# Kernel tuning notes

Hardware: AMD Instinct MI355X
Metric: run time of the kernel (lower is better)

## Reference

```python
import jax, jax.numpy as jnp
import numpy as np

H, C = 8, 32          # heads, per-head channels
N, E = 100000, 1600000
NEG_SLOPE = 0.2
LN_EPS = 1e-5


def layer_norm(x, g, b):
    mu = jnp.mean(x, axis=-1, keepdims=True)
    var = jnp.mean((x - mu) ** 2, axis=-1, keepdims=True)
    return (x - mu) * jax.lax.rsqrt(var + LN_EPS) * g + b


def setup_inputs() -> dict:
    key = jax.random.key(0)
    ks = jax.random.split(key, 8)
    x = jax.random.normal(ks[0], (N, C), dtype=jnp.float32)
    edge_index = jax.random.randint(ks[1], (2, E), 0, N, dtype=jnp.int64)
    s = 1.0 / np.sqrt(C)
    W_gat = jax.random.normal(ks[2], (C, H * C), dtype=jnp.float32) * s
    att_src = jax.random.normal(ks[3], (H, C), dtype=jnp.float32) * s
    att_dst = jax.random.normal(ks[4], (H, C), dtype=jnp.float32) * s
    bias_gat = jnp.zeros((C,), jnp.float32)
    w1 = jax.random.normal(ks[5], (C, 128), dtype=jnp.float32) * s
    b1 = jnp.zeros((128,), jnp.float32)
    w2 = jax.random.normal(ks[6], (128, C), dtype=jnp.float32) / np.sqrt(128)
    b2 = jnp.zeros((C,), jnp.float32)
    g1 = jnp.ones((C,), jnp.float32); be1 = jnp.zeros((C,), jnp.float32)
    g2 = jnp.ones((C,), jnp.float32); be2 = jnp.zeros((C,), jnp.float32)
    return dict(x=x, edge_index=edge_index, W_gat=W_gat, att_src=att_src,
                att_dst=att_dst, bias_gat=bias_gat, w1=w1, b1=b1, w2=w2,
                b2=b2, g1=g1, be1=be1, g2=g2, be2=be2)


def gat_conv(x, edge_index, W_gat, att_src, att_dst, bias_gat):
    n = x.shape[0]
    # add self loops (PyG default)
    loops = jnp.arange(n, dtype=edge_index.dtype)
    ei = jnp.concatenate([edge_index, jnp.stack([loops, loops])], axis=1)
    src, dst = ei[0], ei[1]
    xp = (x @ W_gat).reshape(n, H, C)                      # [N,H,C]
    a_src = jnp.einsum('nhc,hc->nh', xp, att_src)          # [N,H]
    a_dst = jnp.einsum('nhc,hc->nh', xp, att_dst)
    alpha = jax.nn.leaky_relu(a_src[src] + a_dst[dst], NEG_SLOPE)  # [E',H]
    # segment softmax over incoming edges of each dst node
    m = jax.ops.segment_max(alpha, dst, num_segments=n)
    ea = jnp.exp(alpha - m[dst])
    denom = jax.ops.segment_sum(ea, dst, num_segments=n)
    attn = ea / (denom[dst] + 1e-16)                       # [E',H]
    msg = xp[src] * attn[..., None]                        # [E',H,C]
    out = jax.ops.segment_sum(msg, dst, num_segments=n)    # [N,H,C]
    return out.mean(axis=1) + bias_gat                     # concat=False -> head mean


def reference(x, edge_index, W_gat, att_src, att_dst, bias_gat,
              w1, b1, w2, b2, g1, be1, g2, be2):
    h = gat_conv(x, edge_index, W_gat, att_src, att_dst, bias_gat)
    h = layer_norm(h + x, g1, be1)
    ff = jax.nn.relu(h @ w1 + b1) @ w2 + b2
    return layer_norm(ff + h, g2, be2)
```

## Files before the change

### kernel.cpp

```cpp
#include <hip/hip_runtime.h>
#include <hip/hip_fp16.h>
#include <stdint.h>

#define HH 8
#define CC 32
#define HC 256
#define FF 128
#define NEG 0.2f
#define LNEPS 1e-5f

typedef __attribute__((ext_vector_type(8))) short bf16x8;
typedef __attribute__((ext_vector_type(4))) float f32x4;
typedef unsigned short u16;

__device__ inline unsigned bf16r(float f) {
  unsigned u = __float_as_uint(f);
  return (u + 0x7fffu + ((u >> 16) & 1u)) >> 16;
}
__device__ inline float bflo(unsigned w) { return __uint_as_float(w << 16); }
__device__ inline float bfhi(unsigned w) { return __uint_as_float(w & 0xffff0000u); }
__device__ inline float leaky(float v) { return v >= 0.f ? v : NEG * v; }
__device__ inline float h2f(unsigned hbits) {
  return __half2float(__ushort_as_half((unsigned short)hbits));
}
__device__ inline u16 f2h(float f) {
  return __half_as_ushort(__float2half(f));
}
__device__ inline float ub0(unsigned w) { return (float)(w & 0xffu); }
__device__ inline float ub1(unsigned w) { return (float)((w >> 8) & 0xffu); }
__device__ inline float ub2(unsigned w) { return (float)((w >> 16) & 0xffu); }
__device__ inline float ub3(unsigned w) { return (float)(w >> 24); }

__global__ __launch_bounds__(256) void klayout(
    const float* __restrict__ W, const float* __restrict__ atts,
    const float* __restrict__ attd, const float* __restrict__ w1,
    const float* __restrict__ w2,
    u16* __restrict__ Wb, u16* __restrict__ Zb,
    u16* __restrict__ V1b, u16* __restrict__ V2b)
{
  int t = threadIdx.x;
  for (int i = t; i < 16 * 512; i += 256) {
    int j = i & 7, l = (i >> 3) & 63, nb = i >> 9;
    int k = 8 * (l >> 4) + j, c = 16 * nb + (l & 15);
    Wb[i] = (u16)bf16r(W[k * HC + c]);
  }
  for (int i = t; i < 8 * 512; i += 256) {
    int j = i & 7, l = (i >> 3) & 63, kb = i >> 9;
    int k = 32 * kb + 8 * (l >> 4) + j;
    int tc = l & 15;
    float v = 0.f;
    if (tc < 8)  { if ((k >> 5) == tc)     v = atts[tc * 32 + (k & 31)]; }
    else         { if ((k >> 5) == tc - 8) v = attd[(tc - 8) * 32 + (k & 31)]; }
    Zb[i] = (u16)bf16r(v);
  }
  for (int i = t; i < 8 * 512; i += 256) {
    int j = i & 7, l = (i >> 3) & 63, nb = i >> 9;
    int k = 8 * (l >> 4) + j, c = 16 * nb + (l & 15);
    V1b[i] = (u16)bf16r(w1[k * FF + c]);
  }
  for (int i = t; i < 8 * 512; i += 256) {
    int j = i & 7, l = (i >> 3) & 63, kn = i >> 9;
    int kb = kn >> 1, nb2 = kn & 1;
    int k = 32 * kb + 8 * (l >> 4) + j, c = 16 * nb2 + (l & 15);
    V2b[i] = (u16)bf16r(w2[k * CC + c]);
  }
}

__global__ __launch_bounds__(256) void k1m(
    const float* __restrict__ x, const u16* __restrict__ Wb,
    const u16* __restrict__ Zb, const int* __restrict__ ei,
    unsigned* __restrict__ xq8, unsigned* __restrict__ ascp,
    float* __restrict__ a_d, int* __restrict__ deg,
    unsigned* __restrict__ dstr, int n, int e, int nbc)
{
  if ((int)blockIdx.x >= nbc) {
    int i = ((int)blockIdx.x - nbc) * 1024 + (int)threadIdx.x * 4;
    if (i >= e) return;
    const int* dst = ei + e;
    if (i + 3 < e) {
      int4 d4 = *(const int4*)(dst + i);
      unsigned r0 = (unsigned)atomicAdd(&deg[d4.x], 1);
      unsigned r1 = (unsigned)atomicAdd(&deg[d4.y], 1);
      unsigned r2 = (unsigned)atomicAdd(&deg[d4.z], 1);
      unsigned r3 = (unsigned)atomicAdd(&deg[d4.w], 1);
      uint4 o;
      o.x = (unsigned)d4.x | (r0 << 17);
      o.y = (unsigned)d4.y | (r1 << 17);
      o.z = (unsigned)d4.z | (r2 << 17);
      o.w = (unsigned)d4.w | (r3 << 17);
      *(uint4*)(dstr + i) = o;
    } else {
      for (int k = 0; k < 4 && i + k < e; ++k) {
        int d = dst[i + k];
        unsigned r = (unsigned)atomicAdd(&deg[d], 1);
        dstr[i + k] = (unsigned)d | (r << 17);
      }
    }
    return;
  }
  __shared__ u16 lt[4][16 * 264];
  __shared__ float lsc[4][16][8];
  int wid = threadIdx.x >> 6, lane = threadIdx.x & 63;
  int q = lane & 15, g = lane >> 4;
  long node0 = (long)((int)blockIdx.x * 4 + wid) * 16;
  if (node0 + 16 > n) node0 = n - 16;
  u16* L = lt[wid];

  const float* xr = x + (node0 + q) * CC + 8 * g;
  float4 xa = *(const float4*)xr, xb = *(const float4*)(xr + 4);
  bf16x8 af;
  af[0] = (short)bf16r(xa.x); af[1] = (short)bf16r(xa.y);
  af[2] = (short)bf16r(xa.z); af[3] = (short)bf16r(xa.w);
  af[4] = (short)bf16r(xb.x); af[5] = (short)bf16r(xb.y);
  af[6] = (short)bf16r(xb.z); af[7] = (short)bf16r(xb.w);

#pragma unroll
  for (int nb = 0; nb < 16; ++nb) {
    bf16x8 bf = *(const bf16x8*)(Wb + nb * 512 + lane * 8);
    f32x4 acc = {0.f, 0.f, 0.f, 0.f};
    acc = __builtin_amdgcn_mfma_f32_16x16x32_bf16(af, bf, acc, 0, 0, 0);
    int col = 16 * nb + q;
#pragma unroll
    for (int r = 0; r < 4; ++r)
      L[(4 * g + r) * 264 + col] = (u16)bf16r(acc[r]);
  }
  __syncthreads();

  f32x4 az = {0.f, 0.f, 0.f, 0.f};
#pragma unroll
  for (int kb = 0; kb < 8; ++kb) {
    bf16x8 a2 = *(const bf16x8*)(L + q * 264 + kb * 32 + g * 8);
    bf16x8 zb = *(const bf16x8*)(Zb + kb * 512 + lane * 8);
    az = __builtin_amdgcn_mfma_f32_16x16x32_bf16(a2, zb, az, 0, 0, 0);
  }
  int hq = q & 7;
  u16* ascp16 = (u16*)ascp;
  if (q < 8) {
#pragma unroll
    for (int r = 0; r < 4; ++r)
      ascp16[((node0 + 4 * g + r) * HH + hq) * 2] = (u16)bf16r(az[r]);
  } else {
#pragma unroll
    for (int r = 0; r < 4; ++r)
      a_d[(node0 + 4 * g + r) * HH + hq] = az[r];
  }

#pragma unroll
  for (int t2 = 0; t2 < 2; ++t2) {
    int task = t2 * 64 + lane;
    int r = task >> 3, h = task & 7;
    const unsigned* p = (const unsigned*)(L + r * 264 + h * 32);
    float mx = 0.f;
#pragma unroll
    for (int i = 0; i < 16; ++i) {
      unsigned w = p[i];
      mx = fmaxf(mx, fmaxf(fabsf(bflo(w)), fabsf(bfhi(w))));
    }
    float rinv = (mx > 0.f) ? 127.f / mx : 0.f;
    ascp16[((node0 + r) * HH + h) * 2 + 1] = f2h(mx * (1.f / 127.f));
    lsc[wid][r][h] = rinv;
  }
  __syncthreads();

#pragma unroll
  for (int i = 0; i < 16; ++i) {
    int d = i * 64 + lane;
    int r = d >> 6, c = d & 63;
    int h = c >> 3;
    float rv = lsc[wid][r][h];
    const unsigned* p = (const unsigned*)(L + r * 264) + (c << 1);
    unsigned w0 = p[0], w1 = p[1];
    int q0 = __float2int_rn(bflo(w0) * rv);
    int q1 = __float2int_rn(bfhi(w0) * rv);
    int q2 = __float2int_rn(bflo(w1) * rv);
    int q3 = __float2int_rn(bfhi(w1) * rv);
    q0 = min(max(q0, -127), 127) + 128;
    q1 = min(max(q1, -127), 127) + 128;
    q2 = min(max(q2, -127), 127) + 128;
    q3 = min(max(q3, -127), 127) + 128;
    unsigned pk = (unsigned)q0 | ((unsigned)q1 << 8) |
                  ((unsigned)q2 << 16) | ((unsigned)q3 << 24);
    xq8[(node0 + r) * 64 + c] = pk;
  }
}

__global__ __launch_bounds__(256) void kscanA(const int* __restrict__ deg,
                                              int* __restrict__ bsum, int n)
{
  __shared__ int ws[4];
  int t = threadIdx.x;
  int i = (int)blockIdx.x * 1024 + t * 4;
  int4 v = make_int4(0, 0, 0, 0);
  if (i + 3 < n) v = *(const int4*)(deg + i);
  else {
    if (i     < n) v.x = deg[i];
    if (i + 1 < n) v.y = deg[i + 1];
    if (i + 2 < n) v.z = deg[i + 2];
    if (i + 3 < n) v.w = deg[i + 3];
  }
  int s = v.x + v.y + v.z + v.w;
#pragma unroll
  for (int mask = 1; mask < 64; mask <<= 1) s += __shfl_xor(s, mask);
  if ((t & 63) == 0) ws[t >> 6] = s;
  __syncthreads();
  if (t == 0) bsum[blockIdx.x] = ws[0] + ws[1] + ws[2] + ws[3];
}

__global__ __launch_bounds__(1024) void kscanB(int* __restrict__ bsum, int nb)
{
  __shared__ int wsum[16];
  int t = threadIdx.x, lane = t & 63, wid = t >> 6;
  int v = (t < nb) ? bsum[t] : 0;
  int s = v;
#pragma unroll
  for (int d = 1; d < 64; d <<= 1) { int tt = __shfl_up(s, d); if (lane >= d) s += tt; }
  if (lane == 63) wsum[wid] = s;
  __syncthreads();
  if (wid == 0) {
    int w = (lane < 16) ? wsum[lane] : 0;
#pragma unroll
    for (int d = 1; d < 16; d <<= 1) { int tt = __shfl_up(w, d); if (lane >= d) w += tt; }
    if (lane < 16) wsum[lane] = w;
  }
  __syncthreads();
  int excl = s - v + ((wid > 0) ? wsum[wid - 1] : 0);
  if (t < nb) bsum[t] = excl;
}

__global__ __launch_bounds__(256) void kscanC(const int* __restrict__ deg,
                                              const int* __restrict__ bsum,
                                              int* __restrict__ offs, int n)
{
  __shared__ int ws[4];
  int t = threadIdx.x, lane = t & 63, wid = t >> 6;
  int i = (int)blockIdx.x * 1024 + t * 4;
  int4 v = make_int4(0, 0, 0, 0);
  if (i + 3 < n) v = *(const int4*)(deg + i);
  else {
    if (i     < n) v.x = deg[i];
    if (i + 1 < n) v.y = deg[i + 1];
    if (i + 2 < n) v.z = deg[i + 2];
    if (i + 3 < n) v.w = deg[i + 3];
  }
  int tsum = v.x + v.y + v.z + v.w;
  int s = tsum;
#pragma unroll
  for (int d = 1; d < 64; d <<= 1) { int tt = __shfl_up(s, d); if (lane >= d) s += tt; }
  if (lane == 63) ws[wid] = s;
  __syncthreads();
  if (t == 0) {
    int a = ws[0]; ws[0] = 0;
    int b = ws[1]; ws[1] = a; a += b;
    int c = ws[2]; ws[2] = a; a += c;
    ws[3] = a;
  }
  __syncthreads();
  int base = bsum[blockIdx.x] + ws[wid] + (s - tsum);
  if (i     < n) offs[i]     = base; base += v.x;
  if (i + 1 < n) offs[i + 1] = base; base += v.y;
  if (i + 2 < n) offs[i + 2] = base; base += v.z;
  if (i + 3 < n) offs[i + 3] = base;
}

__global__ __launch_bounds__(256) void kscatter(
    const int* __restrict__ ei, const unsigned* __restrict__ dstr, int e,
    const int* __restrict__ offs, int* __restrict__ csr, int n)
{
  int oct = (int)blockIdx.x & 3;
  int nsub = (int)gridDim.x >> 2;
  int sub = (int)blockIdx.x >> 2;
  int nper = (n + 3) >> 2;
  int lo = oct * nper, hi = lo + nper;
  int stride = nsub << 10;
  for (int i = (sub * 256 + (int)threadIdx.x) * 4; i < e; i += stride) {
    if (i + 3 < e) {
      uint4 d4 = *(const uint4*)(dstr + i);
      int4 s4 = *(const int4*)(ei + i);
      int dx = d4.x & 0x1ffff, dy = d4.y & 0x1ffff,
          dz = d4.z & 0x1ffff, dw = d4.w & 0x1ffff;
      if (dx >= lo && dx < hi) csr[offs[dx] + (d4.x >> 17)] = s4.x;
      if (dy >= lo && dy < hi) csr[offs[dy] + (d4.y >> 17)] = s4.y;
      if (dz >= lo && dz < hi) csr[offs[dz] + (d4.z >> 17)] = s4.z;
      if (dw >= lo && dw < hi) csr[offs[dw] + (d4.w >> 17)] = s4.w;
    } else {
      for (int k = 0; k < 4 && i + k < e; ++k) {
        unsigned dv = dstr[i + k];
        int d = dv & 0x1ffff;
        if (d >= lo && d < hi) csr[offs[d] + (dv >> 17)] = ei[i + k];
      }
    }
  }
}

__global__ __launch_bounds__(256) void kagg(
    const int* __restrict__ csr, const int* __restrict__ offs,
    const int* __restrict__ deg,
    const unsigned* __restrict__ ascp, const float* __restrict__ a_d,
    const unsigned* __restrict__ xq8, float* __restrict__ og, int n)
{
  int lane = threadIdx.x & 63;
  int wid  = threadIdx.x >> 6;
  int base = ((int)blockIdx.x * 4 + wid) * 4;
  int eg = lane >> 3, ha = lane & 7;
  int hb = eg;
  int doff = hb * 8 + (lane & 7);

  for (int t = 0; t < 4; ++t) {
    int node = base + t;
    if (node >= n) return;
    int start = offs[node];
    int dg = deg[node];
    unsigned aw_self = ascp[(size_t)node * HH + ha];
    float ad_a  = a_d[(size_t)node * HH + ha];
    float aself = leaky(bflo(aw_self) + ad_a);

    float acc0 = 0.f, acc1 = 0.f, acc2 = 0.f, acc3 = 0.f;
    float dnA = 0.f, osA = 0.f;

    for (int j0 = 0; j0 < dg; j0 += 8) {
      int cnt = dg - j0; if (cnt > 8) cnt = 8;
      int idx = j0 + eg;
      int srcl = 0; float pw = 0.f;
      if (idx < dg) {
        srcl = csr[start + idx];
        unsigned av = ascp[(size_t)srcl * HH + ha];
        float al = leaky(bflo(av) + ad_a);
        float p  = __expf(al - aself);
        pw = p * h2f(av >> 16);
        dnA += p; osA += pw;
      }
      if (cnt == 8) {
#pragma unroll
        for (int j = 0; j < 8; ++j) {
          float wt = __shfl(pw, (j << 3) + hb);
          int s = __shfl(srcl, j << 3);
          unsigned w = xq8[(size_t)s * 64 + doff];
          acc0 = fmaf(ub0(w), wt, acc0);
          acc1 = fmaf(ub1(w), wt, acc1);
          acc2 = fmaf(ub2(w), wt, acc2);
          acc3 = fmaf(ub3(w), wt, acc3);
        }
      } else {
        for (int j = 0; j < cnt; ++j) {
          float wt = __shfl(pw, (j << 3) + hb);
          int s = __shfl(srcl, j << 3);
          unsigned w = xq8[(size_t)s * 64 + doff];
          acc0 = fmaf(ub0(w), wt, acc0);
          acc1 = fmaf(ub1(w), wt, acc1);
          acc2 = fmaf(ub2(w), wt, acc2);
          acc3 = fmaf(ub3(w), wt, acc3);
        }
      }
    }

    float dnH = dnA, osH = osA;
    dnH += __shfl_xor(dnH, 8);  osH += __shfl_xor(osH, 8);
    dnH += __shfl_xor(dnH, 16); osH += __shfl_xor(osH, 16);
    dnH += __shfl_xor(dnH, 32); osH += __shfl_xor(osH, 32);
    float dnB = __shfl(dnH, hb);
    float osB = __shfl(osH, hb);
    float scB = __shfl(h2f(aw_self >> 16), hb);

    {
      unsigned w = xq8[(size_t)node * 64 + doff];
      dnB += 1.f; osB += scB;
      acc0 = fmaf(ub0(w), scB, acc0);
      acc1 = fmaf(ub1(w), scB, acc1);
      acc2 = fmaf(ub2(w), scB, acc2);
      acc3 = fmaf(ub3(w), scB, acc3);
    }

    float corr = -128.f * osB;
    float inv = 0.125f / dnB;
    acc0 = (acc0 + corr) * inv;
    acc1 = (acc1 + corr) * inv;
    acc2 = (acc2 + corr) * inv;
    acc3 = (acc3 + corr) * inv;
#pragma unroll
    for (int mask = 8; mask < 64; mask <<= 1) {
      acc0 += __shfl_xor(acc0, mask);
      acc1 += __shfl_xor(acc1, mask);
      acc2 += __shfl_xor(acc2, mask);
      acc3 += __shfl_xor(acc3, mask);
    }
    if (lane < 8) {
      *(float4*)(og + (size_t)node * CC + lane * 4) =
        make_float4(acc0, acc1, acc2, acc3);
    }
  }
}

__global__ __launch_bounds__(256) void k5m(
    const float* __restrict__ og, const float* __restrict__ x,
    const float* __restrict__ bg,
    const u16* __restrict__ V1b, const u16* __restrict__ V2b,
    const float* __restrict__ b1, const float* __restrict__ b2,
    const float* __restrict__ g1, const float* __restrict__ be1,
    const float* __restrict__ g2, const float* __restrict__ be2,
    float* __restrict__ out, int n)
{
  __shared__ u16   lh[4][16 * 40];
  __shared__ u16   lf[4][16 * 136];
  __shared__ float lo[4][16 * 36];
  int wid = threadIdx.x >> 6, lane = threadIdx.x & 63;
  int q = lane & 15, g = lane >> 4;
  long node0 = (long)((int)blockIdx.x * 4 + wid) * 16;
  if (node0 + 16 > n) node0 = n - 16;
  u16* LH = lh[wid]; u16* LF = lf[wid]; float* LO = lo[wid];

  {
    int row = lane >> 2, off = (lane & 3) * 8;
    const float* o8 = og + (node0 + row) * CC + off;
    const float* x8 = x  + (node0 + row) * CC + off;
    float4 a0 = *(const float4*)o8, a1 = *(const float4*)(o8 + 4);
    float4 c0 = *(const float4*)x8, c1 = *(const float4*)(x8 + 4);
    float4 bg0 = *(const float4*)(bg + off), bg1 = *(const float4*)(bg + off + 4);
    float4 s0 = make_float4(a0.x + c0.x + bg0.x, a0.y + c0.y + bg0.y,
                            a0.z + c0.z + bg0.z, a0.w + c0.w + bg0.w);
    float4 s1 = make_float4(a1.x + c1.x + bg1.x, a1.y + c1.y + bg1.y,
                            a1.z + c1.z + bg1.z, a1.w + c1.w + bg1.w);
    *(float4*)(LO + row * 36 + off)     = s0;
    *(float4*)(LO + row * 36 + off + 4) = s1;
  }
  __syncthreads();

  float hv[32];
  if (lane < 16) {
#pragma unroll
    for (int i = 0; i < 8; ++i) {
      float4 t = *(const float4*)(LO + q * 36 + i * 4);
      hv[4*i] = t.x; hv[4*i+1] = t.y; hv[4*i+2] = t.z; hv[4*i+3] = t.w;
    }
    float mu = 0.f;
#pragma unroll
    for (int c = 0; c < 32; ++c) mu += hv[c];
    mu *= (1.f / 32.f);
    float var = 0.f;
#pragma unroll
    for (int c = 0; c < 32; ++c) { float t = hv[c] - mu; var = fmaf(t, t, var); }
    float rs = rsqrtf(var * (1.f / 32.f) + LNEPS);
#pragma unroll
    for (int c = 0; c < 32; ++c) hv[c] = (hv[c] - mu) * rs * g1[c] + be1[c];
    uint* dst = (uint*)(LH + q * 40);
#pragma unroll
    for (int i = 0; i < 16; ++i)
      dst[i] = bf16r(hv[2*i]) | (bf16r(hv[2*i+1]) << 16);
  }
  __syncthreads();

  bf16x8 ah = *(const bf16x8*)(LH + q * 40 + g * 8);
#pragma unroll
  for (int nb = 0; nb < 8; ++nb) {
    bf16x8 v1 = *(const bf16x8*)(V1b + nb * 512 + lane * 8);
    f32x4 acc = {0.f, 0.f, 0.f, 0.f};
    acc = __builtin_amdgcn_mfma_f32_16x16x32_bf16(ah, v1, acc, 0, 0, 0);
    int col = 16 * nb + q;
    float bias = b1[col];
#pragma unroll
    for (int r = 0; r < 4; ++r) {
      float f = fmaxf(acc[r] + bias, 0.f);
      LF[(4 * g + r) * 136 + col] = (u16)bf16r(f);
    }
  }
  __syncthreads();

  f32x4 a20 = {0.f, 0.f, 0.f, 0.f}, a21 = {0.f, 0.f, 0.f, 0.f};
#pragma unroll
  for (int kb = 0; kb < 4; ++kb) {
    bf16x8 af2 = *(const bf16x8*)(LF + q * 136 + kb * 32 + g * 8);
    bf16x8 v20 = *(const bf16x8*)(V2b + (kb * 2 + 0) * 512 + lane * 8);
    bf16x8 v21 = *(const bf16x8*)(V2b + (kb * 2 + 1) * 512 + lane * 8);
    a20 = __builtin_amdgcn_mfma_f32_16x16x32_bf16(af2, v20, a20, 0, 0, 0);
    a21 = __builtin_amdgcn_mfma_f32_16x16x32_bf16(af2, v21, a21, 0, 0, 0);
  }
  __syncthreads();
#pragma unroll
  for (int r = 0; r < 4; ++r) {
    LO[(4 * g + r) * 36 + q]      = a20[r];
    LO[(4 * g + r) * 36 + 16 + q] = a21[r];
  }
  __syncthreads();

  if (lane < 16) {
    float ov[32];
#pragma unroll
    for (int i = 0; i < 8; ++i) {
      float4 t = *(const float4*)(LO + q * 36 + i * 4);
      ov[4*i] = t.x; ov[4*i+1] = t.y; ov[4*i+2] = t.z; ov[4*i+3] = t.w;
    }
#pragma unroll
    for (int c = 0; c < 32; ++c) ov[c] += b2[c] + hv[c];
    float mu2 = 0.f;
#pragma unroll
    for (int c = 0; c < 32; ++c) mu2 += ov[c];
    mu2 *= (1.f / 32.f);
    float var2 = 0.f;
#pragma unroll
    for (int c = 0; c < 32; ++c) { float t = ov[c] - mu2; var2 = fmaf(t, t, var2); }
    float rs2 = rsqrtf(var2 * (1.f / 32.f) + LNEPS);
    float* op = out + (node0 + q) * CC;
#pragma unroll
    for (int i = 0; i < 8; ++i) {
      float4 o;
      o.x = (ov[4*i]   - mu2) * rs2 * g2[4*i]   + be2[4*i];
      o.y = (ov[4*i+1] - mu2) * rs2 * g2[4*i+1] + be2[4*i+1];
      o.z = (ov[4*i+2] - mu2) * rs2 * g2[4*i+2] + be2[4*i+2];
      o.w = (ov[4*i+3] - mu2) * rs2 * g2[4*i+3] + be2[4*i+3];
      *(float4*)(op + i * 4) = o;
    }
  }
}

extern "C" void kernel_launch(void* const* d_in, const int* in_sizes, int n_in,
                              void* d_out, int out_size, void* d_ws, size_t ws_size,
                              hipStream_t stream)
{
  const float* x    = (const float*)d_in[0];
  const int*   ei   = (const int*)d_in[1];
  const float* W    = (const float*)d_in[2];
  const float* atts = (const float*)d_in[3];
  const float* attd = (const float*)d_in[4];
  const float* bg   = (const float*)d_in[5];
  const float* w1   = (const float*)d_in[6];
  const float* b1   = (const float*)d_in[7];
  const float* w2   = (const float*)d_in[8];
  const float* b2   = (const float*)d_in[9];
  const float* g1   = (const float*)d_in[10];
  const float* be1  = (const float*)d_in[11];
  const float* g2   = (const float*)d_in[12];
  const float* be2  = (const float*)d_in[13];

  int n = in_sizes[0] / CC;
  int e = in_sizes[1] / 2;

  uint8_t* ws = (uint8_t*)d_ws;
  size_t o = 0;
  unsigned* xq8 = (unsigned*)(ws + o); o += (size_t)n * 256;
  unsigned* ascp = (unsigned*)(ws + o); o += (size_t)n * HH * 4;
  float* a_d = (float*)(ws + o); o += (size_t)n * HH * 4;
  float* og  = (float*)(ws + o); o += (size_t)n * CC * 4;
  int* deg    = (int*)(ws + o); o += (size_t)n * 4;
  int* offs   = (int*)(ws + o); o += (size_t)n * 4;
  unsigned* dstr = (unsigned*)(ws + o); o += (size_t)e * 4;
  int* csr    = (int*)(ws + o); o += (size_t)e * 4;
  int* bsum   = (int*)(ws + o); o += 4096;
  u16* Wb  = (u16*)(ws + o); o += 16 * 512 * 2;
  u16* Zb  = (u16*)(ws + o); o += 8 * 512 * 2;
  u16* V1b = (u16*)(ws + o); o += 8 * 512 * 2;
  u16* V2b = (u16*)(ws + o); o += 8 * 512 * 2;

  (void)hipMemsetAsync(deg, 0, (size_t)n * 4, stream);

  int nwaves = (n + 15) / 16;
  int nbc   = (nwaves + 3) / 4;
  int nb_e4 = (e + 1023) / 1024;
  int nb_s  = (n + 1023) / 1024;
  int nb_ag = (n + 15) / 16;

  klayout <<<1, 256, 0, stream>>>(W, atts, attd, w1, w2, Wb, Zb, V1b, V2b);
  k1m     <<<nbc + nb_e4, 256, 0, stream>>>(x, Wb, Zb, ei, xq8, ascp, a_d, deg,
                                            dstr, n, e, nbc);
  kscanA  <<<nb_s, 256, 0, stream>>>(deg, bsum, n);
  kscanB  <<<1, 1024, 0, stream>>>(bsum, nb_s);
  kscanC  <<<nb_s, 256, 0, stream>>>(deg, bsum, offs, n);
  kscatter<<<512, 256, 0, stream>>>(ei, dstr, e, offs, csr, n);
  kagg    <<<nb_ag, 256, 0, stream>>>(csr, offs, deg, ascp, a_d, xq8, og, n);
  k5m     <<<nbc, 256, 0, stream>>>(og, x, bg, V1b, V2b, b1, b2, g1, be1, g2, be2,
                                    (float*)d_out, n);
}
```

Measured before the change: 262.5 us.

## Replicate degree histogram four ways to reduce atomic contention; split edge-count kernel

The degree-count atomics now go to four replicated histograms selected by block index, which is meant to reduce same-address atomic contention. Each edge's packed word now records which replica it used. The scan produces per-replica base offsets plus a total degree, and the scatter uses them to place edges. The histogram work is split out of the fused projection kernel into its own launch, which adds one launch, quadruples the counter memset, and makes the scan read and write four times the data. kagg receives rb (whose first replica row equals the old offsets) and degt.

Measured after the change: 253.3 us. 1.04x faster.

```diff
diff --git a/kernel.cpp b/kernel.cpp
--- a/kernel.cpp
+++ b/kernel.cpp
@@ -66,38 +66,42 @@
   }
 }
 
-__global__ __launch_bounds__(256) void k1m(
+__global__ __launch_bounds__(256) void khist(
+    const int* __restrict__ ei, int e, int n,
+    int* __restrict__ deg4, unsigned* __restrict__ dstr)
+{
+  int r = (int)blockIdx.x & 3;
+  int* dr = deg4 + (size_t)r * n;
+  int i = (int)blockIdx.x * 1024 + (int)threadIdx.x * 4;
+  if (i >= e) return;
+  const int* dst = ei + e;
+  if (i + 3 < e) {
+    int4 d4 = *(const int4*)(dst + i);
+    unsigned r0 = (unsigned)atomicAdd(&dr[d4.x], 1);
+    unsigned r1 = (unsigned)atomicAdd(&dr[d4.y], 1);
+    unsigned r2 = (unsigned)atomicAdd(&dr[d4.z], 1);
+    unsigned r3 = (unsigned)atomicAdd(&dr[d4.w], 1);
+    uint4 o;
+    o.x = (unsigned)d4.x | ((unsigned)r << 17) | (r0 << 19);
+    o.y = (unsigned)d4.y | ((unsigned)r << 17) | (r1 << 19);
+    o.z = (unsigned)d4.z | ((unsigned)r << 17) | (r2 << 19);
+    o.w = (unsigned)d4.w | ((unsigned)r << 17) | (r3 << 19);
+    *(uint4*)(dstr + i) = o;
+  } else {
+    for (int k = 0; k < 4 && i + k < e; ++k) {
+      int d = dst[i + k];
+      unsigned rr = (unsigned)atomicAdd(&dr[d], 1);
+      dstr[i + k] = (unsigned)d | ((unsigned)r << 17) | (rr << 19);
+    }
+  }
+}
+
+__global__ __launch_bounds__(256) void k1c(
     const float* __restrict__ x, const u16* __restrict__ Wb,
-    const u16* __restrict__ Zb, const int* __restrict__ ei,
+    const u16* __restrict__ Zb,
     unsigned* __restrict__ xq8, unsigned* __restrict__ ascp,
-    float* __restrict__ a_d, int* __restrict__ deg,
-    unsigned* __restrict__ dstr, int n, int e, int nbc)
-{
-  if ((int)blockIdx.x >= nbc) {
-    int i = ((int)blockIdx.x - nbc) * 1024 + (int)threadIdx.x * 4;
-    if (i >= e) return;
-    const int* dst = ei + e;
-    if (i + 3 < e) {
-      int4 d4 = *(const int4*)(dst + i);
-      unsigned r0 = (unsigned)atomicAdd(&deg[d4.x], 1);
-      unsigned r1 = (unsigned)atomicAdd(&deg[d4.y], 1);
-      unsigned r2 = (unsigned)atomicAdd(&deg[d4.z], 1);
-      unsigned r3 = (unsigned)atomicAdd(&deg[d4.w], 1);
-      uint4 o;
-      o.x = (unsigned)d4.x | (r0 << 17);
-      o.y = (unsigned)d4.y | (r1 << 17);
-      o.z = (unsigned)d4.z | (r2 << 17);
-      o.w = (unsigned)d4.w | (r3 << 17);
-      *(uint4*)(dstr + i) = o;
-    } else {
-      for (int k = 0; k < 4 && i + k < e; ++k) {
-        int d = dst[i + k];
-        unsigned r = (unsigned)atomicAdd(&deg[d], 1);
-        dstr[i + k] = (unsigned)d | (r << 17);
-      }
-    }
-    return;
-  }
+    float* __restrict__ a_d, int n)
+{
   __shared__ u16 lt[4][16 * 264];
   __shared__ float lsc[4][16][8];
   int wid = threadIdx.x >> 6, lane = threadIdx.x & 63;
@@ -184,21 +188,24 @@
   }
 }
 
-__global__ __launch_bounds__(256) void kscanA(const int* __restrict__ deg,
+__global__ __launch_bounds__(256) void kscanA(const int* __restrict__ deg4,
                                               int* __restrict__ bsum, int n)
 {
   __shared__ int ws[4];
   int t = threadIdx.x;
   int i = (int)blockIdx.x * 1024 + t * 4;
-  int4 v = make_int4(0, 0, 0, 0);
-  if (i + 3 < n) v = *(const int4*)(deg + i);
-  else {
-    if (i     < n) v.x = deg[i];
-    if (i + 1 < n) v.y = deg[i + 1];
-    if (i + 2 < n) v.z = deg[i + 2];
-    if (i + 3 < n) v.w = deg[i + 3];
-  }
-  int s = v.x + v.y + v.z + v.w;
+  int s = 0;
+  if (i + 3 < n) {
+#pragma unroll
+    for (int r = 0; r < 4; ++r) {
+      int4 v = *(const int4*)(deg4 + (size_t)r * n + i);
+      s += v.x + v.y + v.z + v.w;
+    }
+  } else {
+    for (int k = 0; k < 4 && i + k < n; ++k)
+#pragma unroll
+      for (int r = 0; r < 4; ++r) s += deg4[(size_t)r * n + i + k];
+  }
 #pragma unroll
   for (int mask = 1; mask < 64; mask <<= 1) s += __shfl_xor(s, mask);
   if ((t & 63) == 0) ws[t >> 6] = s;
@@ -227,22 +234,36 @@
   if (t < nb) bsum[t] = excl;
 }
 
-__global__ __launch_bounds__(256) void kscanC(const int* __restrict__ deg,
+__global__ __launch_bounds__(256) void kscanC(const int* __restrict__ deg4,
                                               const int* __restrict__ bsum,
-                                              int* __restrict__ offs, int n)
+                                              int* __restrict__ rb,
+                                              int* __restrict__ degt, int n)
 {
   __shared__ int ws[4];
   int t = threadIdx.x, lane = t & 63, wid = t >> 6;
   int i = (int)blockIdx.x * 1024 + t * 4;
-  int4 v = make_int4(0, 0, 0, 0);
-  if (i + 3 < n) v = *(const int4*)(deg + i);
-  else {
-    if (i     < n) v.x = deg[i];
-    if (i + 1 < n) v.y = deg[i + 1];
-    if (i + 2 < n) v.z = deg[i + 2];
-    if (i + 3 < n) v.w = deg[i + 3];
-  }
-  int tsum = v.x + v.y + v.z + v.w;
+  int c0[4] = {0,0,0,0}, c1[4] = {0,0,0,0}, c2[4] = {0,0,0,0}, c3[4] = {0,0,0,0};
+  if (i + 3 < n) {
+    int4 v0 = *(const int4*)(deg4 + 0 * (size_t)n + i);
+    int4 v1 = *(const int4*)(deg4 + 1 * (size_t)n + i);
+    int4 v2 = *(const int4*)(deg4 + 2 * (size_t)n + i);
+    int4 v3 = *(const int4*)(deg4 + 3 * (size_t)n + i);
+    c0[0]=v0.x;c0[1]=v0.y;c0[2]=v0.z;c0[3]=v0.w;
+    c1[0]=v1.x;c1[1]=v1.y;c1[2]=v1.z;c1[3]=v1.w;
+    c2[0]=v2.x;c2[1]=v2.y;c2[2]=v2.z;c2[3]=v2.w;
+    c3[0]=v3.x;c3[1]=v3.y;c3[2]=v3.z;c3[3]=v3.w;
+  } else {
+    for (int k = 0; k < 4 && i + k < n; ++k) {
+      c0[k] = deg4[0 * (size_t)n + i + k];
+      c1[k] = deg4[1 * (size_t)n + i + k];
+      c2[k] = deg4[2 * (size_t)n + i + k];
+      c3[k] = deg4[3 * (size_t)n + i + k];
+    }
+  }
+  int tot[4];
+#pragma unroll
+  for (int k = 0; k < 4; ++k) tot[k] = c0[k] + c1[k] + c2[k] + c3[k];
+  int tsum = tot[0] + tot[1] + tot[2] + tot[3];
   int s = tsum;
 #pragma unroll
   for (int d = 1; d < 64; d <<= 1) { int tt = __shfl_up(s, d); if (lane >= d) s += tt; }
@@ -256,15 +277,23 @@
   }
   __syncthreads();
   int base = bsum[blockIdx.x] + ws[wid] + (s - tsum);
-  if (i     < n) offs[i]     = base; base += v.x;
-  if (i + 1 < n) offs[i + 1] = base; base += v.y;
-  if (i + 2 < n) offs[i + 2] = base; base += v.z;
-  if (i + 3 < n) offs[i + 3] = base;
+#pragma unroll
+  for (int k = 0; k < 4; ++k) {
+    if (i + k < n) {
+      int b0 = base;
+      rb[0 * (size_t)n + i + k] = b0;
+      rb[1 * (size_t)n + i + k] = b0 + c0[k];
+      rb[2 * (size_t)n + i + k] = b0 + c0[k] + c1[k];
+      rb[3 * (size_t)n + i + k] = b0 + c0[k] + c1[k] + c2[k];
+      degt[i + k] = tot[k];
+    }
+    base += tot[k];
+  }
 }
 
 __global__ __launch_bounds__(256) void kscatter(
     const int* __restrict__ ei, const unsigned* __restrict__ dstr, int e,
-    const int* __restrict__ offs, int* __restrict__ csr, int n)
+    const int* __restrict__ rb, int* __restrict__ csr, int n)
 {
   int oct = (int)blockIdx.x & 3;
   int nsub = (int)gridDim.x >> 2;
@@ -278,15 +307,20 @@
       int4 s4 = *(const int4*)(ei + i);
       int dx = d4.x & 0x1ffff, dy = d4.y & 0x1ffff,
           dz = d4.z & 0x1ffff, dw = d4.w & 0x1ffff;
-      if (dx >= lo && dx < hi) csr[offs[dx] + (d4.x >> 17)] = s4.x;
-      if (dy >= lo && dy < hi) csr[offs[dy] + (d4.y >> 17)] = s4.y;
-      if (dz >= lo && dz < hi) csr[offs[dz] + (d4.z >> 17)] = s4.z;
-      if (dw >= lo && dw < hi) csr[offs[dw] + (d4.w >> 17)] = s4.w;
+      if (dx >= lo && dx < hi)
+        csr[rb[(size_t)((d4.x >> 17) & 3) * n + dx] + (d4.x >> 19)] = s4.x;
+      if (dy >= lo && dy < hi)
+        csr[rb[(size_t)((d4.y >> 17) & 3) * n + dy] + (d4.y >> 19)] = s4.y;
+      if (dz >= lo && dz < hi)
+        csr[rb[(size_t)((d4.z >> 17) & 3) * n + dz] + (d4.z >> 19)] = s4.z;
+      if (dw >= lo && dw < hi)
+        csr[rb[(size_t)((d4.w >> 17) & 3) * n + dw] + (d4.w >> 19)] = s4.w;
     } else {
       for (int k = 0; k < 4 && i + k < e; ++k) {
         unsigned dv = dstr[i + k];
         int d = dv & 0x1ffff;
-        if (d >= lo && d < hi) csr[offs[d] + (dv >> 17)] = ei[i + k];
+        if (d >= lo && d < hi)
+          csr[rb[(size_t)((dv >> 17) & 3) * n + d] + (dv >> 19)] = ei[i + k];
       }
     }
   }
@@ -294,7 +328,7 @@
 
 __global__ __launch_bounds__(256) void kagg(
     const int* __restrict__ csr, const int* __restrict__ offs,
-    const int* __restrict__ deg,
+    const int* __restrict__ degt,
     const unsigned* __restrict__ ascp, const float* __restrict__ a_d,
     const unsigned* __restrict__ xq8, float* __restrict__ og, int n)
 {
@@ -309,7 +343,7 @@
     int node = base + t;
     if (node >= n) return;
     int start = offs[node];
-    int dg = deg[node];
+    int dg = degt[node];
     unsigned aw_self = ascp[(size_t)node * HH + ha];
     float ad_a  = a_d[(size_t)node * HH + ha];
     float aself = leaky(bflo(aw_self) + ad_a);
@@ -539,8 +573,9 @@
   unsigned* ascp = (unsigned*)(ws + o); o += (size_t)n * HH * 4;
   float* a_d = (float*)(ws + o); o += (size_t)n * HH * 4;
   float* og  = (float*)(ws + o); o += (size_t)n * CC * 4;
-  int* deg    = (int*)(ws + o); o += (size_t)n * 4;
-  int* offs   = (int*)(ws + o); o += (size_t)n * 4;
+  int* deg4   = (int*)(ws + o); o += (size_t)n * 4 * 4;
+  int* rb     = (int*)(ws + o); o += (size_t)n * 4 * 4;
+  int* degt   = (int*)(ws + o); o += (size_t)n * 4;
   unsigned* dstr = (unsigned*)(ws + o); o += (size_t)e * 4;
   int* csr    = (int*)(ws + o); o += (size_t)e * 4;
   int* bsum   = (int*)(ws + o); o += 4096;
@@ -549,7 +584,7 @@
   u16* V1b = (u16*)(ws + o); o += 8 * 512 * 2;
   u16* V2b = (u16*)(ws + o); o += 8 * 512 * 2;
 
-  (void)hipMemsetAsync(deg, 0, (size_t)n * 4, stream);
+  (void)hipMemsetAsync(deg4, 0, (size_t)n * 4 * 4, stream);
 
   int nwaves = (n + 15) / 16;
   int nbc   = (nwaves + 3) / 4;
@@ -557,14 +592,14 @@
   int nb_s  = (n + 1023) / 1024;
   int nb_ag = (n + 15) / 16;
 
+  khist   <<<nb_e4, 256, 0, stream>>>(ei, e, n, deg4, dstr);
   klayout <<<1, 256, 0, stream>>>(W, atts, attd, w1, w2, Wb, Zb, V1b, V2b);
-  k1m     <<<nbc + nb_e4, 256, 0, stream>>>(x, Wb, Zb, ei, xq8, ascp, a_d, deg,
-                                            dstr, n, e, nbc);
-  kscanA  <<<nb_s, 256, 0, stream>>>(deg, bsum, n);
+  k1c     <<<nbc, 256, 0, stream>>>(x, Wb, Zb, xq8, ascp, a_d, n);
+  kscanA  <<<nb_s, 256, 0, stream>>>(deg4, bsum, n);
   kscanB  <<<1, 1024, 0, stream>>>(bsum, nb_s);
-  kscanC  <<<nb_s, 256, 0, stream>>>(deg, bsum, offs, n);
-  kscatter<<<512, 256, 0, stream>>>(ei, dstr, e, offs, csr, n);
-  kagg    <<<nb_ag, 256, 0, stream>>>(csr, offs, deg, ascp, a_d, xq8, og, n);
+  kscanC  <<<nb_s, 256, 0, stream>>>(deg4, bsum, rb, degt, n);
+  kscatter<<<512, 256, 0, stream>>>(ei, dstr, e, rb, csr, n);
+  kagg    <<<nb_ag, 256, 0, stream>>>(csr, rb, degt, ascp, a_d, xq8, og, n);
   k5m     <<<nbc, 256, 0, stream>>>(og, x, bg, V1b, V2b, b1, b2, g1, be1, g2, be2,
                                     (float*)d_out, n);
 }
```
